# Performance work log

Measured on AMD Instinct MI355X. Metric: run time of the kernel, lower is better.

## Reference

```python
import jax, jax.numpy as jnp
import numpy as np

N_NODES = 100000
N_EDGES = 1600000
N_HOPS = 3
D_FEAT = 128
D_HID = 256
NUM_GRAPHS = 64


def setup_inputs() -> dict:
    key = jax.random.key(0)
    ks = jax.random.split(key, 8)
    x = jax.random.normal(ks[0], (N_NODES, D_FEAT), dtype=jnp.float32)
    edge_index = jax.random.randint(ks[1], (N_HOPS, 2, N_EDGES), 0, N_NODES, dtype=jnp.int64)
    edge_weight = jax.random.uniform(ks[2], (N_HOPS, N_EDGES), dtype=jnp.float32)
    batch = jnp.sort(jax.random.randint(ks[3], (N_NODES,), 0, NUM_GRAPHS, dtype=jnp.int64))
    w1 = jax.random.normal(ks[4], (D_FEAT, D_HID), dtype=jnp.float32) * (1.0 / np.sqrt(D_FEAT))
    b1 = jnp.zeros((D_HID,), dtype=jnp.float32)
    w2 = jax.random.normal(ks[5], (D_HID, D_FEAT), dtype=jnp.float32) * (1.0 / np.sqrt(D_HID))
    b2 = jnp.zeros((D_FEAT,), dtype=jnp.float32)
    prop_w = jnp.ones((N_HOPS + 1,), dtype=jnp.float32)
    return {"x": x, "edge_index": edge_index, "edge_weight": edge_weight,
            "batch": batch, "w1": w1, "b1": b1, "w2": w2, "b2": b2, "prop_w": prop_w}


def reference(x, edge_index, edge_weight, batch, w1, b1, w2, b2, prop_w):
    n = x.shape[0]
    # MLP: dropout is identity in eval mode
    h = jax.nn.relu(x @ w1 + b1)          # [N, hid]
    h = h @ w2 + b2                        # [N, feat]
    # prop_weight: weighted sum over hops; hop i uses edge_index[layers[i]-1]
    acc = prop_w[0] * h
    for i in range(edge_index.shape[0]):
        src = edge_index[i, 0]             # x_j source nodes
        dst = edge_index[i, 1]             # aggregation targets
        msg = edge_weight[i][:, None] * h[src]              # [E, feat]
        agg = jax.ops.segment_sum(msg, dst, num_segments=n)  # [N, feat]
        acc = acc + prop_w[i + 1] * agg
    # sum over hop dim already folded into acc; global_add_pool over graphs
    pooled = jax.ops.segment_sum(acc, batch, num_segments=NUM_GRAPHS)  # [G, feat]
    # original returns log_softmax of pooled features (lin3 output is unused)
    return jax.nn.log_softmax(pooled, axis=1)
```

## Files before the change

### kernel.cpp

```cpp
#include <hip/hip_runtime.h>
#include <hip/hip_bf16.h>


#define N_NODES 100000
#define N_EDGES 1600000
#define N_HOPS 3
#define D_HID 256
#define N_GRAPHS 64

#define CHUNK 32
#define NCHUNK 3125
#define FG 512

#define NB 625
#define RB 160
#define NSH 4
#define CAP 2400
#define SGRID 500
#define SB 1024
#define I4PB 2400
#define NI4H 400000

#define CT_OFF    0u
#define REC_OFF   12800000u
#define SPART_OFF REC_OFF
#define SMALL_OFF 36800000u
#define CUR_OFF   SMALL_OFF
#define TG_OFF    (SMALL_OFF + 16384u)
#define SSUM_OFF  (SMALL_OFF + 32768u)
#define W1P_OFF   (SMALL_OFF + 131072u)

typedef __attribute__((ext_vector_type(4))) float f32x4;
typedef __attribute__((ext_vector_type(8))) short s16x8;
typedef __attribute__((ext_vector_type(4))) int i32x4;
typedef __attribute__((ext_vector_type(4))) float fv4;

__device__ __forceinline__ unsigned short f2bf_rne(float f) {
    union { float f; unsigned u; } v; v.f = f;
    unsigned r = v.u + 0x7FFFu + ((v.u >> 16) & 1u);
    return (unsigned short)(r >> 16);
}
__device__ __forceinline__ float bf2f(unsigned short s) {
    union { float f; unsigned u; } v; v.u = ((unsigned)s) << 16;
    return v.f;
}
__device__ __forceinline__ unsigned pk_rne(float lo, float hi) {
    return ((unsigned)f2bf_rne(hi) << 16) | (unsigned)f2bf_rne(lo);
}

__global__ __launch_bounds__(256) void w1_prep(const float* __restrict__ w1,
                                               unsigned short* __restrict__ w1p) {
    int f = blockIdx.x * 256 + threadIdx.x;
    int t = f >> 4, fr = f & 15, nt = fr >> 2, ks = fr & 3;
    int w = t >> 6, l = t & 63, q = l >> 4, c = l & 15;
    s16x8 v;
#pragma unroll
    for (int j = 0; j < 8; j++)
        v[j] = (short)f2bf_rne(w1[(size_t)(32 * ks + 8 * q + j) * 256 + w * 64 + 16 * nt + c]);
    *(s16x8*)&w1p[(size_t)f * 8] = v;
}

__global__ __launch_bounds__(SB) void scatter_kernel(
    const int* __restrict__ ei, const float* __restrict__ ew,
    const int* __restrict__ batch, const float* __restrict__ pw,
    unsigned* __restrict__ cursors, unsigned* __restrict__ records) {
    __shared__ unsigned cnt[NB], basearr[NB];
    const int tid = threadIdx.x;
    const int sh = blockIdx.x & (NSH - 1);
    const int i40 = blockIdx.x * I4PB;

    if (tid < NB) cnt[tid] = 0u;
    __syncthreads();

    const float pw1 = pw[1], pw2 = pw[2], pw3 = pw[3];

    unsigned rec[12], bkt[12];
#pragma unroll
    for (int k = 0; k < 3; k++) {
        int idx = tid + k * SB;
        if (idx < I4PB) {
            int i4 = i40 + idx;
            unsigned hop = (unsigned)i4 / NI4H;
            int r4 = i4 - (int)hop * NI4H;
            const i32x4* sp4 = (const i32x4*)(ei + (size_t)hop * 2 * N_EDGES);
            i32x4 s = __builtin_nontemporal_load(sp4 + r4);
            i32x4 d = __builtin_nontemporal_load(sp4 + NI4H + r4);
            fv4 wv = __builtin_nontemporal_load((const fv4*)(ew + (size_t)hop * N_EDGES) + r4);
            float pwh = hop == 0 ? pw1 : (hop == 1 ? pw2 : pw3);
#pragma unroll
            for (int j = 0; j < 4; j++) {
                unsigned b = (unsigned)s[j] / RB;
                bkt[k * 4 + j] = b;
                rec[k * 4 + j] = ((unsigned)f2bf_rne(pwh * wv[j]) << 16) |
                                 (unsigned)(((unsigned)s[j] - b * RB) * 64 + batch[d[j]]);
                atomicAdd(&cnt[b], 1u);
            }
        } else {
#pragma unroll
            for (int j = 0; j < 4; j++) bkt[k * 4 + j] = 0xFFFFFFFFu;
        }
    }
    __syncthreads();
    if (tid < NB) {
        unsigned c = cnt[tid];
        basearr[tid] = c ? atomicAdd(&cursors[sh * NB + tid], c) : 0u;
        cnt[tid] = 0u;
    }
    __syncthreads();
#pragma unroll
    for (int k = 0; k < 12; k++) {
        if (bkt[k] != 0xFFFFFFFFu) {
            unsigned o = atomicAdd(&cnt[bkt[k]], 1u);
            records[((size_t)sh * NB + bkt[k]) * CAP + basearr[bkt[k]] + o] = rec[k];
        }
    }
}

__global__ __launch_bounds__(512) void phaseB_kernel(
    const int* __restrict__ batch, const float* __restrict__ pw,
    const unsigned* __restrict__ cursors, const unsigned* __restrict__ records,
    unsigned short* __restrict__ ct, float* __restrict__ tg) {
    __shared__ float tile[RB * 65];
    const int tid = threadIdx.x;
    const int b = blockIdx.x;

    for (int i = tid; i < RB * 65; i += 512) tile[i] = 0.f;
    __syncthreads();

    if (tid < RB) atomicAdd(&tile[tid * 65 + batch[b * RB + tid]], pw[0]);

    for (int sh = 0; sh < NSH; sh++) {
        unsigned n = cursors[sh * NB + b];
        const unsigned* rp = records + ((size_t)sh * NB + b) * CAP;
        unsigned n4 = n >> 2;
        for (unsigned i = tid; i < n4; i += 512) {
            uint4 r4 = *(const uint4*)(rp + 4 * i);
            unsigned m0 = r4.x & 0x3FFFu, m1 = r4.y & 0x3FFFu;
            unsigned m2 = r4.z & 0x3FFFu, m3 = r4.w & 0x3FFFu;
            atomicAdd(&tile[m0 + (m0 >> 6)], bf2f((unsigned short)(r4.x >> 16)));
            atomicAdd(&tile[m1 + (m1 >> 6)], bf2f((unsigned short)(r4.y >> 16)));
            atomicAdd(&tile[m2 + (m2 >> 6)], bf2f((unsigned short)(r4.z >> 16)));
            atomicAdd(&tile[m3 + (m3 >> 6)], bf2f((unsigned short)(r4.w >> 16)));
        }
        unsigned i = 4 * n4 + tid;
        if (i < n) {
            unsigned r = rp[i];
            unsigned m = r & 0x3FFFu;
            atomicAdd(&tile[m + (m >> 6)], bf2f((unsigned short)(r >> 16)));
        }
    }
    __syncthreads();

    if (tid < 256) {
        const int gt = tid >> 6, l = tid & 63, q = l >> 4, c = l & 15;
        for (int cc = 0; cc < 5; cc++) {
            s16x8 v;
#pragma unroll
            for (int j = 0; j < 8; j++)
                v[j] = (short)f2bf_rne(tile[(cc * 32 + 8 * q + j) * 65 + 16 * gt + c]);
            *(s16x8*)&ct[(((size_t)(b * 5 + cc) * 4 + gt) * 64 + l) * 8] = v;
        }
    }
    if (tid < 64) {
        float sum = 0.f;
        for (int s = 0; s < RB; s++) sum += tile[s * 65 + tid];
        atomicAdd(&tg[tid], sum);
    }
}

__global__ __launch_bounds__(256, 2) void fused_kernel(
    const float* __restrict__ x,
    const unsigned short* __restrict__ w1p,
    const float* __restrict__ b1,
    const unsigned short* __restrict__ ct,
    unsigned short* __restrict__ s_part) {

    __shared__ __align__(16) unsigned short Ut[256 * 40];
    __shared__ __align__(16) unsigned short x_lds[32 * 136];
    __shared__ __align__(16) unsigned short ct_lds[2048];

    const int tid = threadIdx.x;
    const int w = tid >> 6, l = tid & 63, q = l >> 4, c = l & 15;
    const int wcol = w * 64;
    const int sr = tid >> 3, sk = (tid & 7) * 16;

    s16x8 w1f[4][4];
    {
        const s16x8* wp = (const s16x8*)(w1p + (size_t)tid * 128);
#pragma unroll
        for (int nt = 0; nt < 4; nt++)
#pragma unroll
            for (int ks = 0; ks < 4; ks++)
                w1f[nt][ks] = wp[nt * 4 + ks];
    }

    float bias[4];
#pragma unroll
    for (int nt = 0; nt < 4; nt++) bias[nt] = b1[wcol + 16 * nt + c];

    f32x4 sacc[4][4];
#pragma unroll
    for (int gt = 0; gt < 4; gt++)
#pragma unroll
        for (int nt = 0; nt < 4; nt++) sacc[gt][nt] = (f32x4)0.f;

    uint4 xp0, xp1;
    s16x8 ctp;

#define PREF(CI)                                                              \
    {                                                                         \
        const float4* p = (const float4*)&x[(size_t)((CI) * 32 + sr) * 128 + sk]; \
        float4 v0 = p[0], v1 = p[1], v2 = p[2], v3 = p[3];                    \
        xp0.x = pk_rne(v0.x, v0.y); xp0.y = pk_rne(v0.z, v0.w);               \
        xp0.z = pk_rne(v1.x, v1.y); xp0.w = pk_rne(v1.z, v1.w);               \
        xp1.x = pk_rne(v2.x, v2.y); xp1.y = pk_rne(v2.z, v2.w);               \
        xp1.z = pk_rne(v3.x, v3.y); xp1.w = pk_rne(v3.z, v3.w);               \
        ctp = *(const s16x8*)&ct[(size_t)(CI) * 2048 + tid * 8];              \
    }

    int ci = blockIdx.x;
    if (ci < NCHUNK) PREF(ci);

    for (; ci < NCHUNK; ci += FG) {
        *(uint4*)&x_lds[sr * 136 + sk] = xp0;
        *(uint4*)&x_lds[sr * 136 + sk + 8] = xp1;
        *(s16x8*)&ct_lds[tid * 8] = ctp;
        __syncthreads();

        s16x8 af[2][4], ctf[4];
#pragma unroll
        for (int mt = 0; mt < 2; mt++)
#pragma unroll
            for (int ks = 0; ks < 4; ks++)
                af[mt][ks] = *(const s16x8*)&x_lds[(16 * mt + c) * 136 + 32 * ks + 8 * q];
#pragma unroll
        for (int gt = 0; gt < 4; gt++)
            ctf[gt] = *(const s16x8*)&ct_lds[(gt * 64 + l) * 8];
        __syncthreads();

        if (ci + FG < NCHUNK) PREF(ci + FG);

        f32x4 u[2][4];
#pragma unroll
        for (int mt = 0; mt < 2; mt++)
#pragma unroll
            for (int nt = 0; nt < 4; nt++) {
                f32x4 a; a[0] = a[1] = a[2] = a[3] = bias[nt];
                u[mt][nt] = a;
            }
#pragma unroll
        for (int ks = 0; ks < 4; ks++)
#pragma unroll
            for (int mt = 0; mt < 2; mt++)
#pragma unroll
                for (int nt = 0; nt < 4; nt++)
                    u[mt][nt] = __builtin_amdgcn_mfma_f32_16x16x32_bf16(
                        af[mt][ks], w1f[nt][ks], u[mt][nt], 0, 0, 0);

#pragma unroll
        for (int mt = 0; mt < 2; mt++)
#pragma unroll
            for (int nt = 0; nt < 4; nt++) {
                f32x4 v = u[mt][nt];
                uint2 d;
                d.x = pk_rne(fmaxf(v[0], 0.f), fmaxf(v[1], 0.f));
                d.y = pk_rne(fmaxf(v[2], 0.f), fmaxf(v[3], 0.f));
                *(uint2*)&Ut[(wcol + 16 * nt + c) * 40 + 16 * mt + 4 * q] = d;
            }

#pragma unroll
        for (int nt = 0; nt < 4; nt++) {
            s16x8 uf = *(const s16x8*)&Ut[(wcol + 16 * nt + c) * 40 + 8 * q];
#pragma unroll
            for (int gt = 0; gt < 4; gt++)
                sacc[gt][nt] = __builtin_amdgcn_mfma_f32_16x16x32_bf16(
                    ctf[gt], uf, sacc[gt][nt], 0, 0, 0);
        }
    }
#undef PREF

    unsigned short* my = s_part + (size_t)blockIdx.x * (64 * 256);
#pragma unroll
    for (int gt = 0; gt < 4; gt++)
#pragma unroll
        for (int nt = 0; nt < 4; nt++)
#pragma unroll
            for (int r = 0; r < 4; r++)
                my[(16 * gt + 4 * q + r) * 256 + wcol + 16 * nt + c] =
                    f2bf_rne(sacc[gt][nt][r]);
}

__global__ __launch_bounds__(256) void reduce_kernel(const unsigned short* __restrict__ s_part,
                                                     float* __restrict__ s_sum) {
    __shared__ float red[4][64];
    const int l = threadIdx.x & 63, p = threadIdx.x >> 6;
    const int e = blockIdx.x * 64 + l;
    float a0 = 0.f, a1 = 0.f, a2 = 0.f, a3 = 0.f;
    for (int b = p * (FG / 4); b < (p + 1) * (FG / 4); b += 4) {
        a0 += bf2f(s_part[(size_t)(b + 0) * 16384 + e]);
        a1 += bf2f(s_part[(size_t)(b + 1) * 16384 + e]);
        a2 += bf2f(s_part[(size_t)(b + 2) * 16384 + e]);
        a3 += bf2f(s_part[(size_t)(b + 3) * 16384 + e]);
    }
    red[p][l] = (a0 + a1) + (a2 + a3);
    __syncthreads();
    if (p == 0) s_sum[e] = (red[0][l] + red[1][l]) + (red[2][l] + red[3][l]);
}

__global__ void finalize_kernel(const float* __restrict__ s,
                                const float* __restrict__ t,
                                const float* __restrict__ w2,
                                const float* __restrict__ b2,
                                float* __restrict__ out) {
    __shared__ float red[128];
    const int g = blockIdx.x;
    const int f = threadIdx.x;

    float acc = t[g] * b2[f];
    for (int k = 0; k < D_HID; k++)
        acc += s[(size_t)g * 256 + k] * w2[(size_t)k * 128 + f];

    red[f] = acc;
    __syncthreads();
    for (int off = 64; off > 0; off >>= 1) {
        if (f < off) red[f] = fmaxf(red[f], red[f + off]);
        __syncthreads();
    }
    float mx = red[0];
    __syncthreads();
    red[f] = expf(acc - mx);
    __syncthreads();
    for (int off = 64; off > 0; off >>= 1) {
        if (f < off) red[f] += red[f + off];
        __syncthreads();
    }
    float lse = logf(red[0]);
    out[(size_t)g * 128 + f] = acc - mx - lse;
}

extern "C" void kernel_launch(void* const* d_in, const int* in_sizes, int n_in,
                              void* d_out, int out_size, void* d_ws, size_t ws_size,
                              hipStream_t stream) {
    const float* x     = (const float*)d_in[0];
    const int*   ei    = (const int*)d_in[1];
    const float* ew    = (const float*)d_in[2];
    const int*   batch = (const int*)d_in[3];
    const float* w1    = (const float*)d_in[4];
    const float* b1    = (const float*)d_in[5];
    const float* w2    = (const float*)d_in[6];
    const float* b2    = (const float*)d_in[7];
    const float* pw    = (const float*)d_in[8];
    float* out = (float*)d_out;

    unsigned short* ctp     = (unsigned short*)((char*)d_ws + CT_OFF);
    unsigned*       records = (unsigned*)((char*)d_ws + REC_OFF);
    unsigned short* s_part  = (unsigned short*)((char*)d_ws + SPART_OFF);
    unsigned*       cursors = (unsigned*)((char*)d_ws + CUR_OFF);
    float*          tgp     = (float*)((char*)d_ws + TG_OFF);
    float*          s_sum   = (float*)((char*)d_ws + SSUM_OFF);
    unsigned short* w1pp    = (unsigned short*)((char*)d_ws + W1P_OFF);

    hipMemsetAsync(cursors, 0, NSH * NB * sizeof(unsigned), stream);
    hipMemsetAsync(tgp, 0, 64 * sizeof(float), stream);

    w1_prep<<<dim3(16), 256, 0, stream>>>(w1, w1pp);
    scatter_kernel<<<dim3(SGRID), SB, 0, stream>>>(
        ei, ew, batch, pw, cursors, records);
    phaseB_kernel<<<dim3(NB), 512, 0, stream>>>(batch, pw, cursors, records, ctp, tgp);
    fused_kernel<<<dim3(FG), 256, 0, stream>>>(x, w1pp, b1, ctp, s_part);
    reduce_kernel<<<dim3(256), 256, 0, stream>>>(s_part, s_sum);
    finalize_kernel<<<dim3(64), 128, 0, stream>>>(s_sum, tgp, w2, b2, out);
}
```

Measured before the change: 254.4 us.

## Stage scatter records in LDS for vectorized writes and compress batch to u8

Scatter records are now first placed into a per-block shared-memory staging buffer. Each bucket's slice is padded to a multiple of four with zero-weight records, so it can be flushed to global memory with 16-byte stores instead of scattered 4-byte writes. A prep kernel also converts the batch ids to a byte array, which shrinks the footprint of the random batch[dst] gather. The costs are more LDS per block (possible occupancy loss), extra prefix-scan and barrier work, and padded records that later stages must read.

```diff
diff --git a/kernel.cpp b/kernel.cpp
--- a/kernel.cpp
+++ b/kernel.cpp
@@ -20,8 +20,10 @@
 #define SB 1024
 #define I4PB 2400
 #define NI4H 400000
+#define STAGE_W 11475
 
 #define CT_OFF    0u
+#define BU8_OFF   0u
 #define REC_OFF   12800000u
 #define SPART_OFF REC_OFF
 #define SMALL_OFF 36800000u
@@ -48,24 +50,40 @@
     return ((unsigned)f2bf_rne(hi) << 16) | (unsigned)f2bf_rne(lo);
 }
 
-__global__ __launch_bounds__(256) void w1_prep(const float* __restrict__ w1,
-                                               unsigned short* __restrict__ w1p) {
-    int f = blockIdx.x * 256 + threadIdx.x;
-    int t = f >> 4, fr = f & 15, nt = fr >> 2, ks = fr & 3;
-    int w = t >> 6, l = t & 63, q = l >> 4, c = l & 15;
-    s16x8 v;
-#pragma unroll
-    for (int j = 0; j < 8; j++)
-        v[j] = (short)f2bf_rne(w1[(size_t)(32 * ks + 8 * q + j) * 256 + w * 64 + 16 * nt + c]);
-    *(s16x8*)&w1p[(size_t)f * 8] = v;
+__global__ __launch_bounds__(256) void prep_kernel(const float* __restrict__ w1,
+                                                   unsigned short* __restrict__ w1p,
+                                                   const int* __restrict__ batch,
+                                                   unsigned char* __restrict__ bu8) {
+    if (blockIdx.x < 16) {
+        int f = blockIdx.x * 256 + threadIdx.x;
+        int t = f >> 4, fr = f & 15, nt = fr >> 2, ks = fr & 3;
+        int w = t >> 6, l = t & 63, q = l >> 4, c = l & 15;
+        s16x8 v;
+#pragma unroll
+        for (int j = 0; j < 8; j++)
+            v[j] = (short)f2bf_rne(w1[(size_t)(32 * ks + 8 * q + j) * 256 + w * 64 + 16 * nt + c]);
+        *(s16x8*)&w1p[(size_t)f * 8] = v;
+    } else {
+        int i = (blockIdx.x - 16) * 1024 + threadIdx.x * 4;
+        if (i < N_NODES) {
+            int4 v = *(const int4*)&batch[i];
+            uchar4 o;
+            o.x = (unsigned char)v.x; o.y = (unsigned char)v.y;
+            o.z = (unsigned char)v.z; o.w = (unsigned char)v.w;
+            *(uchar4*)&bu8[i] = o;
+        }
+    }
 }
 
 __global__ __launch_bounds__(SB) void scatter_kernel(
     const int* __restrict__ ei, const float* __restrict__ ew,
-    const int* __restrict__ batch, const float* __restrict__ pw,
+    const unsigned char* __restrict__ bu8, const float* __restrict__ pw,
     unsigned* __restrict__ cursors, unsigned* __restrict__ records) {
-    __shared__ unsigned cnt[NB], basearr[NB];
+    __shared__ unsigned cnt[NB], basearr[NB], lbase[NB], ccnt[NB];
+    __shared__ unsigned wtot[16];
+    __shared__ unsigned stage[STAGE_W];
     const int tid = threadIdx.x;
+    const int lane = tid & 63, wid = tid >> 6;
     const int sh = blockIdx.x & (NSH - 1);
     const int i40 = blockIdx.x * I4PB;
 
@@ -92,7 +110,7 @@
                 unsigned b = (unsigned)s[j] / RB;
                 bkt[k * 4 + j] = b;
                 rec[k * 4 + j] = ((unsigned)f2bf_rne(pwh * wv[j]) << 16) |
-                                 (unsigned)(((unsigned)s[j] - b * RB) * 64 + batch[d[j]]);
+                                 (unsigned)(((unsigned)s[j] - b * RB) * 64 + (unsigned)bu8[d[j]]);
                 atomicAdd(&cnt[b], 1u);
             }
         } else {
@@ -101,17 +119,57 @@
         }
     }
     __syncthreads();
+
+    unsigned pcv = 0;
     if (tid < NB) {
-        unsigned c = cnt[tid];
-        basearr[tid] = c ? atomicAdd(&cursors[sh * NB + tid], c) : 0u;
+        unsigned cc = cnt[tid];
+        ccnt[tid] = cc;
+        pcv = (cc + 3u) & ~3u;
+        basearr[tid] = pcv ? atomicAdd(&cursors[sh * NB + tid], pcv) : 0u;
         cnt[tid] = 0u;
     }
-    __syncthreads();
+    unsigned inc = pcv;
+#pragma unroll
+    for (int d = 1; d < 64; d <<= 1) {
+        unsigned u = __shfl_up(inc, d, 64);
+        if (lane >= d) inc += u;
+    }
+    if (lane == 63) wtot[wid] = inc;
+    __syncthreads();
+    if (tid < 16) {
+        unsigned wv = wtot[tid];
+        unsigned winc = wv;
+#pragma unroll
+        for (int d = 1; d < 16; d <<= 1) {
+            unsigned u = __shfl_up(winc, d, 16);
+            if ((tid & 15) >= d) winc += u;
+        }
+        wtot[tid] = winc - wv;
+    }
+    __syncthreads();
+    if (tid < NB) {
+        unsigned lb = inc - pcv + wtot[wid];
+        lbase[tid] = lb;
+        for (unsigned i = ccnt[tid]; i < pcv; i++) stage[lb + i] = 0u;
+    }
+    __syncthreads();
+
 #pragma unroll
     for (int k = 0; k < 12; k++) {
         if (bkt[k] != 0xFFFFFFFFu) {
             unsigned o = atomicAdd(&cnt[bkt[k]], 1u);
-            records[((size_t)sh * NB + bkt[k]) * CAP + basearr[bkt[k]] + o] = rec[k];
+            stage[lbase[bkt[k]] + o] = rec[k];
+        }
+    }
+    __syncthreads();
+
+    if (tid < NB) {
+        unsigned pc = (ccnt[tid] + 3u) & ~3u;
+        unsigned lb = lbase[tid];
+        unsigned* dst = records + ((size_t)sh * NB + tid) * CAP + basearr[tid];
+        for (unsigned i = 0; i < pc; i += 4) {
+            uint4 v = *(const uint4*)&stage[lb + i];
+            *(uint4*)&dst[i] = v;
         }
     }
 }
@@ -353,6 +411,7 @@
     float* out = (float*)d_out;
 
     unsigned short* ctp     = (unsigned short*)((char*)d_ws + CT_OFF);
+    unsigned char*  bu8     = (unsigned char*)((char*)d_ws + BU8_OFF);
     unsigned*       records = (unsigned*)((char*)d_ws + REC_OFF);
     unsigned short* s_part  = (unsigned short*)((char*)d_ws + SPART_OFF);
     unsigned*       cursors = (unsigned*)((char*)d_ws + CUR_OFF);
@@ -363,9 +422,9 @@
     hipMemsetAsync(cursors, 0, NSH * NB * sizeof(unsigned), stream);
     hipMemsetAsync(tgp, 0, 64 * sizeof(float), stream);
 
-    w1_prep<<<dim3(16), 256, 0, stream>>>(w1, w1pp);
+    prep_kernel<<<dim3(114), 256, 0, stream>>>(w1, w1pp, batch, bu8);
     scatter_kernel<<<dim3(SGRID), SB, 0, stream>>>(
-        ei, ew, batch, pw, cursors, records);
+        ei, ew, bu8, pw, cursors, records);
     phaseB_kernel<<<dim3(NB), 512, 0, stream>>>(batch, pw, cursors, records, ctp, tgp);
     fused_kernel<<<dim3(FG), 256, 0, stream>>>(x, w1pp, b1, ctp, s_part);
     reduce_kernel<<<dim3(256), 256, 0, stream>>>(s_part, s_sum);
```

Result: faster. 241.9 us (-4.9%).
